# Kernel tuning notes

Hardware: AMD Instinct MI355X
Metric: run time of the kernel (lower is better)

Reference implementation:

```python
import jax, jax.numpy as jnp
import numpy as np

N_NODES = 50000   # item_num + num_users
N_EDGES = 600000
ITEM_NUM = 40000
N_USERS = 10000
D = 128           # embed_size == hidden_size
BS = 512
L = 10            # max_seq_len
N_POS = 200


def setup_inputs() -> dict:
    key = jax.random.key(0)
    ks = jax.random.split(key, 26)
    stdv = 1.0 / np.sqrt(D)
    u = lambda k, shp: jax.random.uniform(k, shp, jnp.float32, -stdv, stdv)
    return {
        "user": jax.random.randint(ks[0], (BS, 1), 0, N_USERS, dtype=jnp.int32),
        "seq": jax.random.randint(ks[1], (BS, L), 0, ITEM_NUM, dtype=jnp.int32),
        "mask": jnp.ones((BS, L), jnp.int32),
        "seq_len": jax.random.randint(ks[2], (BS,), 1, L + 1, dtype=jnp.int32),
        "pos_idx": jax.random.randint(ks[3], (BS, L), 0, N_POS, dtype=jnp.int32),
        "edge_src": jax.random.randint(ks[4], (N_EDGES,), 0, N_NODES, dtype=jnp.int32),
        "edge_dst": jax.random.randint(ks[5], (N_EDGES,), 0, N_NODES, dtype=jnp.int32),
        "item_num": ITEM_NUM,
        # learned parameters (torch Linear weights stored as (in, out) so y = x @ W + b)
        "v2e": u(ks[6], (N_NODES, D)),
        "pos_w": u(ks[7], (N_POS, D)),
        "W_self": u(ks[8], (D, D)),       # SAGEConv fc_self
        "W_neigh": u(ks[9], (D, D)),      # SAGEConv fc_neigh
        "b_sage": u(ks[10], (D,)),
        "w1": u(ks[11], (2 * D, D)),
        "w2": u(ks[12], (D, 1)),
        "glu1_w": u(ks[13], (D, D)),
        "glu1_b": u(ks[14], (D,)),
        "glu2_w": u(ks[15], (D, D)),
        "w3": u(ks[16], (D, D)),
        "w4": u(ks[17], (D, 1)),
        "glu3_w": u(ks[18], (D, D)),
        "glu3_b": u(ks[19], (D,)),
        "glu4_w": u(ks[20], (D, D)),
        "wc_w": u(ks[21], (2 * D, 1)),    # sigmoid_concat Linear
        "wc_b": u(ks[22], (1,)),
    }


def reference(user, seq, mask, seq_len, pos_idx, edge_src, edge_dst, item_num,
              v2e, pos_w, W_self, W_neigh, b_sage, w1, w2, glu1_w, glu1_b,
              glu2_w, w3, w4, glu3_w, glu3_b, glu4_w, wc_w, wc_b):
    N = v2e.shape[0]
    E = edge_src.shape[0]
    # --- SAGEConv('mean') over full graph (dropout is identity in eval) ---
    agg = jax.ops.segment_sum(v2e[edge_src], edge_dst, num_segments=N)      # [N,D]
    deg = jax.ops.segment_sum(jnp.ones((E,), v2e.dtype), edge_dst, num_segments=N)
    neigh = agg / jnp.maximum(deg, 1.0)[:, None]
    h1 = jax.nn.relu(v2e @ W_self + neigh @ W_neigh + b_sage)               # [N,D]

    uidx = user + item_num                                                  # [bs,1]
    item_e = (h1[seq] + v2e[seq]) * 0.5                                     # [bs,L,D]
    user_e = (h1[uidx] + v2e[uidx]) * 0.5                                   # [bs,1,D]
    seq_emb = user_e[:, 0, :]                                               # squeeze(1)

    m = mask.astype(v2e.dtype)[..., None]                                   # [bs,L,1]
    # --- compute_hidden_vector: position-aware soft attention pooling ---
    pos_e = pos_w[pos_idx]                                                  # [bs,L,D]
    avg = (item_e * m).sum(1) / m.sum(1)                                    # [bs,D]
    hs = avg[:, None, :]                                                    # broadcast over L
    nh = jnp.tanh(jnp.concatenate([pos_e, item_e], -1) @ w1)
    nh = jax.nn.sigmoid(nh @ glu1_w + glu1_b + hs @ glu2_w)
    beta = (nh @ w2) * m                                                    # [bs,L,1]
    sess_vec = (beta * item_e).sum(1)                                       # [bs,D]

    # --- sess_user_vector: user-conditioned pooling ---
    nh2 = jnp.tanh(item_e @ w3)
    nh2 = jax.nn.sigmoid(nh2 @ glu3_w + glu3_b + user_e @ glu4_w)
    beta2 = (nh2 @ w4) * m
    sess_user = (beta2 * item_e).sum(1)                                     # [bs,D]

    alpha = jax.nn.sigmoid(jnp.concatenate([sess_vec, sess_user], 1) @ wc_w + wc_b)
    seq_emb = seq_emb + alpha * sess_vec + (1.0 - alpha) * sess_user

    scores = seq_emb @ v2e[1:].T                                            # [bs, N-1]
    return scores
```

## Files before the change

### kernel.cpp

```cpp
#include <hip/hip_runtime.h>
#include <hip/hip_bf16.h>

#define N_NODES 50000
#define N_EDGES 600000
#define D 128
#define BS 512
#define L 10
#define MAXS (BS*L + BS)
#define NOUT 49999
#define NTILES 3125

#define W1T 0
#define W3T 32768
#define G1T 49152
#define G2T 65536
#define G3T 81920
#define G4T 98304
#define WT_ELEMS 114688

typedef __attribute__((ext_vector_type(8))) short bf16x8;
typedef __attribute__((ext_vector_type(4))) float f32x4;

__device__ __forceinline__ unsigned short f2bf(float f){
  union { float f; unsigned int i; } v; v.f = f;
  unsigned int i = v.i;
  return (unsigned short)((i + 0x7fffu + ((i >> 16) & 1u)) >> 16);
}
__device__ __forceinline__ float sigm(float x){ return 1.f/(1.f+__expf(-x)); }
__device__ __forceinline__ float tanh_f(float x){
  x = fminf(fmaxf(x, -15.f), 15.f);
  float e = __expf(2.f*x);
  return (e-1.f)/(e+1.f);
}

__global__ void k_mark(const int* __restrict__ seq, const int* __restrict__ user,
                       const int* __restrict__ item_num, int* __restrict__ map){
  int i = blockIdx.x*256 + threadIdx.x;
  if (i < BS*L) { map[seq[i]] = 1; }
  else if (i < BS*L + BS) { map[user[i - BS*L] + item_num[0]] = 1; }
}

__global__ void k_compact(int* __restrict__ map, int* __restrict__ invmap, int* __restrict__ counters){
  int n = blockIdx.x*256 + threadIdx.x;
  if (n < N_NODES && map[n]) {
    int s = atomicAdd(&counters[0], 1);
    map[n] = s + 2;
    invmap[s] = n;
  }
}

__global__ void k_count(const int* __restrict__ edst, const int* __restrict__ map,
                        int* __restrict__ scount){
  for (int e = blockIdx.x*blockDim.x + threadIdx.x; e < N_EDGES; e += gridDim.x*blockDim.x){
    int mv = map[edst[e]];
    if (mv >= 2) atomicAdd(&scount[mv - 2], 1);
  }
}

__global__ void k_scan(const int* __restrict__ scount, int* __restrict__ soffs){
  __shared__ int part[1024];
  int t = threadIdx.x;
  int base = t*6;
  int loc[6]; int sum = 0;
  #pragma unroll
  for (int j=0;j<6;j++){ int idx = base+j; int c = (idx < MAXS) ? scount[idx] : 0; loc[j]=sum; sum+=c; }
  part[t] = sum; __syncthreads();
  for (int off=1; off<1024; off<<=1){
    int v = (t>=off) ? part[t-off] : 0; __syncthreads();
    part[t] += v; __syncthreads();
  }
  int ex = (t>0) ? part[t-1] : 0;
  #pragma unroll
  for (int j=0;j<6;j++){ int idx = base+j; if (idx < MAXS) soffs[idx] = ex + loc[j]; }
}

__global__ void k_scatter(const int* __restrict__ esrc, const int* __restrict__ edst,
                          const int* __restrict__ map, const int* __restrict__ soffs,
                          int* __restrict__ cursor, int* __restrict__ bucket){
  for (int e = blockIdx.x*blockDim.x + threadIdx.x; e < N_EDGES; e += gridDim.x*blockDim.x){
    int mv = map[edst[e]];
    if (mv >= 2){
      int slot = mv - 2;
      int pos = soffs[slot] + atomicAdd(&cursor[slot], 1);
      bucket[pos] = esrc[e];
    }
  }
}

__global__ void k_neigh(const float* __restrict__ v2e, const int* __restrict__ bucket,
                        const int* __restrict__ soffs, const int* __restrict__ scount,
                        const int* __restrict__ counters, float* __restrict__ neigh){
  int s = blockIdx.x; int t = threadIdx.x;
  if (s >= counters[0]) return;
  int cnt = scount[s]; int off = soffs[s];
  float acc = 0.f;
  for (int j=0;j<cnt;j++){
    int src = bucket[off+j];
    acc += v2e[(size_t)src*D + t];
  }
  neigh[(size_t)s*D + t] = acc / fmaxf((float)cnt, 1.0f);
}

#define SL8 8
__global__ __launch_bounds__(128) void k_h1(const float* __restrict__ v2e,
                     const float* __restrict__ neigh, const int* __restrict__ invmap,
                     const int* __restrict__ counters, const float* __restrict__ Wself,
                     const float* __restrict__ Wneigh, const float* __restrict__ bsage,
                     float* __restrict__ h1c){
  __shared__ float vv[SL8][D];
  __shared__ float nn[SL8][D];
  int t = threadIdx.x;
  int nslots = counters[0];
  int sb = blockIdx.x*SL8;
  for (int i=0;i<SL8;i++){
    int s = sb+i;
    if (s < nslots){
      int node = invmap[s];
      vv[i][t] = v2e[(size_t)node*D + t];
      nn[i][t] = neigh[(size_t)s*D + t];
    }
  }
  __syncthreads();
  float bias = bsage[t];
  float acc[SL8];
  #pragma unroll
  for (int i=0;i<SL8;i++) acc[i] = bias;
  for (int k=0;k<D;k++){
    float ws = Wself[k*D + t];
    float wn = Wneigh[k*D + t];
    #pragma unroll
    for (int i=0;i<SL8;i++) acc[i] += vv[i][k]*ws + nn[i][k]*wn;
  }
  for (int i=0;i<SL8;i++){
    int s = sb+i;
    if (s < nslots) h1c[(size_t)s*D + t] = fmaxf(acc[i], 0.f);
  }
}

__global__ __launch_bounds__(256) void k_prep(const float* __restrict__ w1,
    const float* __restrict__ w3, const float* __restrict__ g1,
    const float* __restrict__ g2, const float* __restrict__ g3,
    const float* __restrict__ g4, unsigned short* __restrict__ wT){
  int bid = blockIdx.x, tid = threadIdx.x;
  if (bid < 128){
    int e = bid*256 + tid;
    int k = e >> 7, n = e & 127;
    wT[W1T + n*256 + k] = f2bf(w1[e]);
  } else {
    int mm = (bid - 128) >> 6;
    int e = ((bid - 128) & 63)*256 + tid;
    int k = e >> 7, n = e & 127;
    const float* src = (mm==0)? w3 : (mm==1)? g1 : (mm==2)? g2 : (mm==3)? g3 : g4;
    int dst = (mm==0)? W3T : (mm==1)? G1T : (mm==2)? G2T : (mm==3)? G3T : G4T;
    wT[dst + n*128 + k] = f2bf(src[e]);
  }
}

__global__ __launch_bounds__(128) void k4a(const int* __restrict__ user, const int* __restrict__ seq,
    const int* __restrict__ mask, const int* __restrict__ pos_idx, const int* __restrict__ item_num,
    const int* __restrict__ map, const float* __restrict__ h1c, const float* __restrict__ v2e,
    const float* __restrict__ pos_w, float* __restrict__ ie, float* __restrict__ ue,
    unsigned short* __restrict__ Xcat, unsigned short* __restrict__ AU){
  int b = blockIdx.x, t = threadIdx.x;
  float av = 0.f, msum = 0.f;
  for (int l=0;l<L;l++){
    int node = seq[b*L+l];
    int slot = map[node]-2;
    float v = 0.5f*(h1c[(size_t)slot*D+t] + v2e[(size_t)node*D+t]);
    ie[(size_t)(b*L+l)*D+t] = v;
    Xcat[(size_t)(b*L+l)*256 + 128 + t] = f2bf(v);
    int p = pos_idx[b*L+l];
    Xcat[(size_t)(b*L+l)*256 + t] = f2bf(pos_w[(size_t)p*D+t]);
    float m = (float)mask[b*L+l];
    av += v*m; msum += m;
  }
  AU[(size_t)b*D+t] = f2bf(av/msum);
  int unode = user[b]+item_num[0];
  int uslot = map[unode]-2;
  float uv = 0.5f*(h1c[(size_t)uslot*D+t] + v2e[(size_t)unode*D+t]);
  ue[(size_t)b*D+t] = uv;
  AU[(size_t)(512+b)*D+t] = f2bf(uv);
}

__global__ __launch_bounds__(256) void k4bc(const unsigned short* __restrict__ Xcat,
    const unsigned short* __restrict__ AU, const unsigned short* __restrict__ wT,
    unsigned short* __restrict__ nh1, unsigned short* __restrict__ nh2,
    float* __restrict__ g24){
  int wv = threadIdx.x>>6, lane = threadIdx.x&63;
  int r = lane&15, q = lane>>4;
  if (blockIdx.x < 320){
    int mt = blockIdx.x;
    const bf16x8* Arow = (const bf16x8*)(Xcat + (size_t)(mt*16+r)*256 + q*8);
    bf16x8 a[8];
    #pragma unroll
    for (int kf=0;kf<8;kf++) a[kf] = Arow[kf*4];
    #pragma unroll
    for (int i=0;i<2;i++){
      int nt = wv + 4*i;
      const bf16x8* Brow = (const bf16x8*)(wT + W1T + (size_t)(nt*16+r)*256 + q*8);
      f32x4 acc = {0.f,0.f,0.f,0.f};
      #pragma unroll
      for (int kf=0;kf<8;kf++)
        acc = __builtin_amdgcn_mfma_f32_16x16x32_bf16(a[kf], Brow[kf*4], acc, 0,0,0);
      #pragma unroll
      for (int g=0; g<4; g++)
        nh1[(size_t)(mt*16 + q*4 + g)*128 + nt*16 + r] = f2bf(tanh_f(acc[g]));
    }
    #pragma unroll
    for (int i=0;i<2;i++){
      int nt = wv + 4*i;
      const bf16x8* Brow = (const bf16x8*)(wT + W3T + (size_t)(nt*16+r)*128 + q*8);
      f32x4 acc = {0.f,0.f,0.f,0.f};
      #pragma unroll
      for (int kf=0;kf<4;kf++)
        acc = __builtin_amdgcn_mfma_f32_16x16x32_bf16(a[4+kf], Brow[kf*4], acc, 0,0,0);
      #pragma unroll
      for (int g=0; g<4; g++)
        nh2[(size_t)(mt*16 + q*4 + g)*128 + nt*16 + r] = f2bf(tanh_f(acc[g]));
    }
  } else {
    int mt = blockIdx.x - 320;
    const unsigned short* Bbase = wT + ((mt*16 >= 512) ? G4T : G2T);
    const bf16x8* Arow = (const bf16x8*)(AU + (size_t)(mt*16+r)*128 + q*8);
    bf16x8 a[4];
    #pragma unroll
    for (int kf=0;kf<4;kf++) a[kf] = Arow[kf*4];
    #pragma unroll
    for (int i=0;i<2;i++){
      int nt = wv + 4*i;
      const bf16x8* Brow = (const bf16x8*)(Bbase + (size_t)(nt*16+r)*128 + q*8);
      f32x4 acc = {0.f,0.f,0.f,0.f};
      #pragma unroll
      for (int kf=0;kf<4;kf++)
        acc = __builtin_amdgcn_mfma_f32_16x16x32_bf16(a[kf], Brow[kf*4], acc, 0,0,0);
      #pragma unroll
      for (int g=0; g<4; g++)
        g24[(size_t)(mt*16 + q*4 + g)*128 + nt*16 + r] = acc[g];
    }
  }
}

__global__ __launch_bounds__(256) void k4d(const unsigned short* __restrict__ nh1,
    const unsigned short* __restrict__ nh2, const unsigned short* __restrict__ wT,
    const float* __restrict__ glu1_b, const float* __restrict__ glu3_b,
    const float* __restrict__ g24, const float* __restrict__ w2, const float* __restrict__ w4,
    float* __restrict__ beta1, float* __restrict__ beta2){
  __shared__ float sb[4][2][16];
  int mt = blockIdx.x;
  int wv = threadIdx.x>>6, lane = threadIdx.x&63;
  int r = lane&15, q = lane>>4;
  int bidx[4];
  #pragma unroll
  for (int g=0; g<4; g++) bidx[g] = (mt*16 + q*4 + g)/10;
  const bf16x8* A1 = (const bf16x8*)(nh1 + (size_t)(mt*16+r)*128 + q*8);
  const bf16x8* A2 = (const bf16x8*)(nh2 + (size_t)(mt*16+r)*128 + q*8);
  bf16x8 a1[4], a2[4];
  #pragma unroll
  for (int kf=0;kf<4;kf++){ a1[kf] = A1[kf*4]; a2[kf] = A2[kf*4]; }
  float accum0[4] = {0.f,0.f,0.f,0.f};
  float accum1[4] = {0.f,0.f,0.f,0.f};
  #pragma unroll
  for (int i=0;i<2;i++){
    int nt = wv + 4*i;
    int col = nt*16 + r;
    {
      const bf16x8* Brow = (const bf16x8*)(wT + G1T + (size_t)col*128 + q*8);
      f32x4 acc = {0.f,0.f,0.f,0.f};
      #pragma unroll
      for (int kf=0;kf<4;kf++)
        acc = __builtin_amdgcn_mfma_f32_16x16x32_bf16(a1[kf], Brow[kf*4], acc, 0,0,0);
      float gb = glu1_b[col], wc = w2[col];
      #pragma unroll
      for (int g=0; g<4; g++){
        float S = acc[g] + gb + g24[(size_t)bidx[g]*128 + col];
        accum0[g] += sigm(S)*wc;
      }
    }
    {
      const bf16x8* Brow = (const bf16x8*)(wT + G3T + (size_t)col*128 + q*8);
      f32x4 acc = {0.f,0.f,0.f,0.f};
      #pragma unroll
      for (int kf=0;kf<4;kf++)
        acc = __builtin_amdgcn_mfma_f32_16x16x32_bf16(a2[kf], Brow[kf*4], acc, 0,0,0);
      float gb = glu3_b[col], wc = w4[col];
      #pragma unroll
      for (int g=0; g<4; g++){
        float S = acc[g] + gb + g24[(size_t)(512 + bidx[g])*128 + col];
        accum1[g] += sigm(S)*wc;
      }
    }
  }
  #pragma unroll
  for (int g=0; g<4; g++){
    float v0 = accum0[g], v1 = accum1[g];
    v0 += __shfl_xor(v0,1,64); v0 += __shfl_xor(v0,2,64); v0 += __shfl_xor(v0,4,64); v0 += __shfl_xor(v0,8,64);
    v1 += __shfl_xor(v1,1,64); v1 += __shfl_xor(v1,2,64); v1 += __shfl_xor(v1,4,64); v1 += __shfl_xor(v1,8,64);
    accum0[g] = v0; accum1[g] = v1;
  }
  if (r == 0){
    #pragma unroll
    for (int g=0; g<4; g++){
      sb[wv][0][q*4+g] = accum0[g];
      sb[wv][1][q*4+g] = accum1[g];
    }
  }
  __syncthreads();
  if (threadIdx.x < 32){
    int m = threadIdx.x>>4, row = threadIdx.x&15;
    float s = sb[0][m][row]+sb[1][m][row]+sb[2][m][row]+sb[3][m][row];
    if (m) beta2[mt*16+row] = s; else beta1[mt*16+row] = s;
  }
}

__global__ __launch_bounds__(128) void k4e(const int* __restrict__ mask,
    const float* __restrict__ beta1, const float* __restrict__ beta2,
    const float* __restrict__ ie, const float* __restrict__ ue,
    const float* __restrict__ wc_w, const float* __restrict__ wc_b,
    unsigned short* __restrict__ semb){
  __shared__ float red[2];
  __shared__ float alphaS;
  int b = blockIdx.x, t = threadIdx.x;
  float sv = 0.f, su = 0.f;
  #pragma unroll
  for (int l=0;l<L;l++){
    float m = (float)mask[b*L+l];
    float b1 = beta1[b*L+l]*m, b2 = beta2[b*L+l]*m;
    float v = ie[(size_t)(b*L+l)*D+t];
    sv += b1*v; su += b2*v;
  }
  float partial = sv*wc_w[t] + su*wc_w[D+t];
  #pragma unroll
  for (int off=32; off; off>>=1) partial += __shfl_down(partial, off, 64);
  if ((t&63)==0) red[t>>6] = partial;
  __syncthreads();
  if (t==0) alphaS = sigm(red[0]+red[1]+wc_b[0]);
  __syncthreads();
  float al = alphaS;
  semb[(size_t)b*D+t] = f2bf(ue[(size_t)b*D+t] + al*sv + (1.f-al)*su);
}

__global__ __launch_bounds__(256) void k_scores(const unsigned short* __restrict__ A,
                                                const float* __restrict__ v2e,
                                                float* __restrict__ out){
  int tid = threadIdx.x;
  int wv = tid >> 6, lane = tid & 63;
  int q = lane >> 4, r = lane & 15;
  int ntile = blockIdx.x*4 + wv;
  int n = ntile*16 + r;
  bool valid = (ntile < NTILES) && (n < NOUT);
  int brow = valid ? (1 + n) : 0;
  const float* Bf = v2e + (size_t)brow*D + q*8;
  bf16x8 b0, b1, b2, b3;
  #pragma unroll
  for (int j=0;j<8;j++){ b0[j] = (short)f2bf(Bf[j]); b1[j] = (short)f2bf(Bf[32+j]);
                         b2[j] = (short)f2bf(Bf[64+j]); b3[j] = (short)f2bf(Bf[96+j]); }
  int mbase = blockIdx.y*8;
  #pragma unroll
  for (int mi=0; mi<8; mi++){
    int mt = mbase + mi;
    const bf16x8* Ap = (const bf16x8*)(A + (size_t)(mt*16 + r)*D + q*8);
    f32x4 acc = {0.f, 0.f, 0.f, 0.f};
    acc = __builtin_amdgcn_mfma_f32_16x16x32_bf16(Ap[0],  b0, acc, 0, 0, 0);
    acc = __builtin_amdgcn_mfma_f32_16x16x32_bf16(Ap[4],  b1, acc, 0, 0, 0);
    acc = __builtin_amdgcn_mfma_f32_16x16x32_bf16(Ap[8],  b2, acc, 0, 0, 0);
    acc = __builtin_amdgcn_mfma_f32_16x16x32_bf16(Ap[12], b3, acc, 0, 0, 0);
    if (valid){
      size_t base = (size_t)(mt*16 + q*4)*NOUT + n;
      out[base]          = acc[0];
      out[base +   NOUT] = acc[1];
      out[base + 2*NOUT] = acc[2];
      out[base + 3*NOUT] = acc[3];
    }
  }
}

extern "C" void kernel_launch(void* const* d_in, const int* in_sizes, int n_in,
                              void* d_out, int out_size, void* d_ws, size_t ws_size,
                              hipStream_t stream) {
  const int* user     = (const int*)d_in[0];
  const int* seq      = (const int*)d_in[1];
  const int* maskp    = (const int*)d_in[2];
  const int* pos_idx  = (const int*)d_in[4];
  const int* esrc     = (const int*)d_in[5];
  const int* edst     = (const int*)d_in[6];
  const int* item_num = (const int*)d_in[7];
  const float* v2e    = (const float*)d_in[8];
  const float* pos_w  = (const float*)d_in[9];
  const float* Wself  = (const float*)d_in[10];
  const float* Wneigh = (const float*)d_in[11];
  const float* bsage  = (const float*)d_in[12];
  const float* w1     = (const float*)d_in[13];
  const float* w2     = (const float*)d_in[14];
  const float* glu1_w = (const float*)d_in[15];
  const float* glu1_b = (const float*)d_in[16];
  const float* glu2_w = (const float*)d_in[17];
  const float* w3     = (const float*)d_in[18];
  const float* w4     = (const float*)d_in[19];
  const float* glu3_w = (const float*)d_in[20];
  const float* glu3_b = (const float*)d_in[21];
  const float* glu4_w = (const float*)d_in[22];
  const float* wc_w   = (const float*)d_in[23];
  const float* wc_b   = (const float*)d_in[24];
  float* out = (float*)d_out;

  char* ws = (char*)d_ws;
  size_t off = 0;
  auto take = [&](size_t n){ size_t o = off; off += (n + 255) & ~(size_t)255; return o; };
  size_t o_cnt    = take(16);
  size_t o_scount = take((size_t)MAXS*4);
  size_t o_cursor = take((size_t)MAXS*4);
  size_t zero_end = off;
  size_t o_soffs  = take((size_t)MAXS*4);
  size_t o_invmap = take((size_t)MAXS*4);
  size_t o_beta1  = take((size_t)BS*L*4);
  size_t o_beta2  = take((size_t)BS*L*4);
  size_t o_semb   = take((size_t)BS*D*2);
  int* counters = (int*)(ws + o_cnt);
  int* scount   = (int*)(ws + o_scount);
  int* cursor   = (int*)(ws + o_cursor);
  int* soffs    = (int*)(ws + o_soffs);
  int* invmap   = (int*)(ws + o_invmap);
  float* beta1  = (float*)(ws + o_beta1);
  float* beta2  = (float*)(ws + o_beta2);
  unsigned short* semb = (unsigned short*)(ws + o_semb);

  char* outb = (char*)d_out;
  size_t to = 84000000;
  auto takeT = [&](size_t n){ size_t o = to; to += (n + 255) & ~(size_t)255; return o; };
  int*            map    = (int*)(outb + takeT((size_t)N_NODES*4));
  int*            bucket = (int*)(outb + takeT((size_t)N_EDGES*4));
  float*          neigh  = (float*)(outb + takeT((size_t)MAXS*D*4));
  float*          h1c    = (float*)(outb + takeT((size_t)MAXS*D*4));
  unsigned short* Xcat   = (unsigned short*)(outb + takeT((size_t)BS*L*256*2));
  unsigned short* nh1    = (unsigned short*)(outb + takeT((size_t)BS*L*D*2));
  unsigned short* nh2    = (unsigned short*)(outb + takeT((size_t)BS*L*D*2));
  unsigned short* AU     = (unsigned short*)(outb + takeT((size_t)2*BS*D*2));
  float*          g24    = (float*)(outb + takeT((size_t)2*BS*D*4));
  float*          ie     = (float*)(outb + takeT((size_t)BS*L*D*4));
  float*          ue     = (float*)(outb + takeT((size_t)BS*D*4));
  unsigned short* wT     = (unsigned short*)(outb + takeT((size_t)WT_ELEMS*2));

  hipMemsetAsync(ws, 0, zero_end, stream);
  hipMemsetAsync(map, 0, (size_t)N_NODES*4, stream);

  k_prep<<<448, 256, 0, stream>>>(w1, w3, glu1_w, glu2_w, glu3_w, glu4_w, wT);
  k_mark<<<(MAXS + 255)/256, 256, 0, stream>>>(seq, user, item_num, map);
  k_compact<<<(N_NODES + 255)/256, 256, 0, stream>>>(map, invmap, counters);
  k_count<<<512, 256, 0, stream>>>(edst, map, scount);
  k_scan<<<1, 1024, 0, stream>>>(scount, soffs);
  k_scatter<<<512, 256, 0, stream>>>(esrc, edst, map, soffs, cursor, bucket);
  k_neigh<<<MAXS, D, 0, stream>>>(v2e, bucket, soffs, scount, counters, neigh);
  k_h1<<<(MAXS + SL8 - 1)/SL8, D, 0, stream>>>(v2e, neigh, invmap, counters, Wself, Wneigh, bsage, h1c);
  k4a<<<BS, D, 0, stream>>>(user, seq, maskp, pos_idx, item_num, map, h1c, v2e, pos_w,
                            ie, ue, Xcat, AU);
  k4bc<<<384, 256, 0, stream>>>(Xcat, AU, wT, nh1, nh2, g24);
  k4d<<<BS*L/16, 256, 0, stream>>>(nh1, nh2, wT, glu1_b, glu3_b, g24, w2, w4, beta1, beta2);
  k4e<<<BS, D, 0, stream>>>(maskp, beta1, beta2, ie, ue, wc_w, wc_b, semb);
  k_scores<<<dim3(782, 4), 256, 0, stream>>>(semb, v2e, out);
}
```

Measured before the change: 337.9 us.

## Store session embeddings in MFMA fragment order and double m-tiles per scores block

k4e now writes the bf16 session embedding in a fragment-major layout, so k_scores can load each A operand as one coalesced 16-byte load per lane instead of strided row reads. The B-operand conversion now uses float4 loads. Each block handles 16 m-tiles, two at a time with independent accumulators, and the grid's y dimension is halved. This reuses the converted v2e fragments across more rows and halves redundant B loads, at the cost of fewer blocks and more registers per thread.

```diff
diff --git a/kernel.cpp b/kernel.cpp
--- a/kernel.cpp
+++ b/kernel.cpp
@@ -336,10 +336,13 @@
   if (t==0) alphaS = sigm(red[0]+red[1]+wc_b[0]);
   __syncthreads();
   float al = alphaS;
-  semb[(size_t)b*D+t] = f2bf(ue[(size_t)b*D+t] + al*sv + (1.f-al)*su);
-}
-
-__global__ __launch_bounds__(256) void k_scores(const unsigned short* __restrict__ A,
+  float val = ue[(size_t)b*D+t] + al*sv + (1.f-al)*su;
+  int mt = b>>4, r = b&15;
+  int kf = t>>5, q = (t>>3)&3, j = t&7;
+  semb[(size_t)((mt*4+kf)*64 + q*16 + r)*8 + j] = f2bf(val);
+}
+
+__global__ __launch_bounds__(256) void k_scores(const unsigned short* __restrict__ Afrag,
                                                 const float* __restrict__ v2e,
                                                 float* __restrict__ out){
   int tid = threadIdx.x;
@@ -349,27 +352,45 @@
   int n = ntile*16 + r;
   bool valid = (ntile < NTILES) && (n < NOUT);
   int brow = valid ? (1 + n) : 0;
-  const float* Bf = v2e + (size_t)brow*D + q*8;
-  bf16x8 b0, b1, b2, b3;
-  #pragma unroll
-  for (int j=0;j<8;j++){ b0[j] = (short)f2bf(Bf[j]); b1[j] = (short)f2bf(Bf[32+j]);
-                         b2[j] = (short)f2bf(Bf[64+j]); b3[j] = (short)f2bf(Bf[96+j]); }
-  int mbase = blockIdx.y*8;
-  #pragma unroll
-  for (int mi=0; mi<8; mi++){
-    int mt = mbase + mi;
-    const bf16x8* Ap = (const bf16x8*)(A + (size_t)(mt*16 + r)*D + q*8);
-    f32x4 acc = {0.f, 0.f, 0.f, 0.f};
-    acc = __builtin_amdgcn_mfma_f32_16x16x32_bf16(Ap[0],  b0, acc, 0, 0, 0);
-    acc = __builtin_amdgcn_mfma_f32_16x16x32_bf16(Ap[4],  b1, acc, 0, 0, 0);
-    acc = __builtin_amdgcn_mfma_f32_16x16x32_bf16(Ap[8],  b2, acc, 0, 0, 0);
-    acc = __builtin_amdgcn_mfma_f32_16x16x32_bf16(Ap[12], b3, acc, 0, 0, 0);
+  const float4* Bf = (const float4*)(v2e + (size_t)brow*D + q*8);
+  bf16x8 b[4];
+  #pragma unroll
+  for (int kf=0; kf<4; kf++){
+    float4 lo = Bf[kf*8];
+    float4 hi = Bf[kf*8 + 1];
+    b[kf][0] = (short)f2bf(lo.x); b[kf][1] = (short)f2bf(lo.y);
+    b[kf][2] = (short)f2bf(lo.z); b[kf][3] = (short)f2bf(lo.w);
+    b[kf][4] = (short)f2bf(hi.x); b[kf][5] = (short)f2bf(hi.y);
+    b[kf][6] = (short)f2bf(hi.z); b[kf][7] = (short)f2bf(hi.w);
+  }
+  const bf16x8* Af = (const bf16x8*)Afrag;
+  int mbase = blockIdx.y*16;
+  for (int u=0; u<8; ++u){
+    int mt0 = mbase + u*2;
+    bf16x8 a0[4], a1[4];
+    #pragma unroll
+    for (int kf=0;kf<4;kf++) a0[kf] = Af[(size_t)(mt0*4+kf)*64 + lane];
+    #pragma unroll
+    for (int kf=0;kf<4;kf++) a1[kf] = Af[(size_t)((mt0+1)*4+kf)*64 + lane];
+    f32x4 acc0 = {0.f,0.f,0.f,0.f};
+    f32x4 acc1 = {0.f,0.f,0.f,0.f};
+    #pragma unroll
+    for (int kf=0;kf<4;kf++)
+      acc0 = __builtin_amdgcn_mfma_f32_16x16x32_bf16(a0[kf], b[kf], acc0, 0,0,0);
+    #pragma unroll
+    for (int kf=0;kf<4;kf++)
+      acc1 = __builtin_amdgcn_mfma_f32_16x16x32_bf16(a1[kf], b[kf], acc1, 0,0,0);
     if (valid){
-      size_t base = (size_t)(mt*16 + q*4)*NOUT + n;
-      out[base]          = acc[0];
-      out[base +   NOUT] = acc[1];
-      out[base + 2*NOUT] = acc[2];
-      out[base + 3*NOUT] = acc[3];
+      size_t base0 = (size_t)(mt0*16 + q*4)*NOUT + n;
+      out[base0]          = acc0[0];
+      out[base0 +   NOUT] = acc0[1];
+      out[base0 + 2*NOUT] = acc0[2];
+      out[base0 + 3*NOUT] = acc0[3];
+      size_t base1 = base0 + (size_t)16*NOUT;
+      out[base1]          = acc1[0];
+      out[base1 +   NOUT] = acc1[1];
+      out[base1 + 2*NOUT] = acc1[2];
+      out[base1 + 3*NOUT] = acc1[3];
     }
   }
 }
@@ -456,5 +477,5 @@
   k4bc<<<384, 256, 0, stream>>>(Xcat, AU, wT, nh1, nh2, g24);
   k4d<<<BS*L/16, 256, 0, stream>>>(nh1, nh2, wT, glu1_b, glu3_b, g24, w2, w4, beta1, beta2);
   k4e<<<BS, D, 0, stream>>>(maskp, beta1, beta2, ie, ue, wc_w, wc_b, semb);
-  k_scores<<<dim3(782, 4), 256, 0, stream>>>(semb, v2e, out);
-}
+  k_scores<<<dim3(782, 2), 256, 0, stream>>>(semb, v2e, out);
+}
```

New measurement: 309.9 us. 8.3% less time.
